# Kernel tuning notes

Measured on AMD Instinct MI355X. Metric: run time of the kernel, lower is better.

Reference implementation:

```python
import jax, jax.numpy as jnp
import numpy as np

H, HEADS, DH = 768, 8, 96
B, NPB = 32, 2048
N, E = B * NPB, B * NPB * 16
K_START = 3  # top-k query-similar start nodes per batch (min(3, nodes))
SCALE = np.float32(1.0 / np.sqrt(DH))


def _ln(x, g, b):
    m = x.mean(-1, keepdims=True)
    v = ((x - m) ** 2).mean(-1, keepdims=True)
    return (x - m) / jnp.sqrt(v + 1e-5) * g + b


def setup_inputs() -> dict:
    key = jax.random.key(0)
    ks = jax.random.split(key, 40)
    s = 0.02
    w = lambda k, sh: jax.random.normal(k, sh, jnp.float32) * s
    query = jax.random.normal(ks[0], (B, H), jnp.float32)
    node_features = jax.random.normal(ks[1], (N, H), jnp.float32)
    # edges only within a graph (contiguous blocks of NPB nodes per batch element)
    bvec = jax.random.randint(ks[2], (E,), 0, B)
    src = bvec * NPB + jax.random.randint(ks[3], (E,), 0, NPB)
    dst = bvec * NPB + jax.random.randint(ks[4], (E,), 0, NPB)
    edge_index = jnp.stack([src, dst]).astype(jnp.int32)
    batch_indices = jnp.repeat(jnp.arange(B, dtype=jnp.int32), NPB)
    inp = dict(query=query, node_features=node_features,
               edge_index=edge_index, batch_indices=batch_indices)
    # GraphReader params: query_projection, MHA in/out proj, LayerNorm
    inp.update(gr_wq=w(ks[5], (H, H)), gr_bq=jnp.zeros((H,)),
               gr_aq_w=w(ks[6], (H, H)), gr_aq_b=jnp.zeros((H,)),
               gr_ak_w=w(ks[7], (H, H)), gr_ak_b=jnp.zeros((H,)),
               gr_av_w=w(ks[8], (H, H)), gr_av_b=jnp.zeros((H,)),
               gr_ao_w=w(ks[9], (H, H)), gr_ao_b=jnp.zeros((H,)),
               gr_ln_g=jnp.ones((H,)), gr_ln_b=jnp.zeros((H,)))
    # PathFinder params: query/node projections, 2-layer path_aggregator, LayerNorm
    inp.update(pf_wq=w(ks[10], (H, H)), pf_bq=jnp.zeros((H,)),
               pf_wn=w(ks[11], (H, H)), pf_bn=jnp.zeros((H,)),
               pf_a1_w=w(ks[12], (H, H)), pf_a1_b=jnp.zeros((H,)),
               pf_a2_w=w(ks[13], (H, H)), pf_a2_b=jnp.zeros((H,)),
               pf_ln_g=jnp.ones((H,)), pf_ln_b=jnp.zeros((H,)))
    # ReasoningFusion (gate) params
    inp.update(fu_gw=w(ks[14], (3 * H, H)), fu_gb=jnp.zeros((H,)),
               fu_pw=w(ks[15], (3 * H, H)), fu_pb=jnp.zeros((H,)),
               fu_ln_g=jnp.ones((H,)), fu_ln_b=jnp.zeros((H,)))
    return inp


def reference(query, node_features, edge_index, batch_indices,
              gr_wq, gr_bq, gr_aq_w, gr_aq_b, gr_ak_w, gr_ak_b, gr_av_w, gr_av_b,
              gr_ao_w, gr_ao_b, gr_ln_g, gr_ln_b,
              pf_wq, pf_bq, pf_wn, pf_bn, pf_a1_w, pf_a1_b, pf_a2_w, pf_a2_b,
              pf_ln_g, pf_ln_b,
              fu_gw, fu_gb, fu_pw, fu_pb, fu_ln_g, fu_ln_b):
    node_b = jnp.arange(B)[:, None] == batch_indices[None, :]  # [B, N] per-batch mask

    # --- GraphReader: single-query masked multi-head attention over each graph ---
    qp = query @ gr_wq + gr_bq
    q = (qp @ gr_aq_w + gr_aq_b).reshape(B, HEADS, DH)
    k = (node_features @ gr_ak_w + gr_ak_b).reshape(N, HEADS, DH)
    v = (node_features @ gr_av_w + gr_av_b).reshape(N, HEADS, DH)
    scores = jnp.einsum('bhd,nhd->bhn', q, k) * SCALE
    scores = jnp.where(node_b[:, None, :], scores, -1e30)
    attn = jax.nn.softmax(scores, axis=-1)
    ctx = jnp.einsum('bhn,nhd->bhd', attn, v).reshape(B, H) @ gr_ao_w + gr_ao_b
    graph_repr = _ln(ctx, gr_ln_g, gr_ln_b)

    # --- PathFinder: top-3 cosine-similar starts, first BFS neighbor per start ---
    qp2 = query @ pf_wq + pf_bq
    nproj = node_features @ pf_wn + pf_bn
    qn = jnp.maximum(jnp.linalg.norm(qp2, axis=-1), 1e-8)
    nn_ = jnp.maximum(jnp.linalg.norm(nproj, axis=-1), 1e-8)
    sim = (qp2 @ nproj.T) / (qn[:, None] * nn_[None, :])
    sim = jnp.where(node_b, sim, -1e30)
    _, starts = jax.lax.top_k(sim, K_START)  # [B, 3] global node ids

    src, dst = edge_index[0], edge_index[1]
    intra = batch_indices[src] == batch_indices[dst]  # BFS keeps same-graph edges
    eids = jnp.where(intra, jnp.arange(E, dtype=jnp.int32), E)
    tgt = jnp.where(intra, src, N)
    # first outgoing edge per node in edge order == first BFS path (start, nbr)
    first_edge = jnp.full((N + 1,), E, jnp.int32).at[tgt].min(eids)[:N]
    has_nb = first_edge < E
    nbr = dst[jnp.minimum(first_edge, E - 1)]

    p_valid = has_nb[starts]  # [B, 3]
    # path length == max_hops (2) -> mean of the two node features (raw features)
    p_feat = (node_features[starts] + node_features[nbr[starts]]) * 0.5  # [B,3,H]
    cnt = p_valid.sum(-1)
    mean_paths = (p_feat * p_valid[..., None].astype(p_feat.dtype)).sum(1) \
                 / jnp.maximum(cnt, 1).astype(p_feat.dtype)[:, None]
    agg = jax.nn.relu(mean_paths @ pf_a1_w + pf_a1_b) @ pf_a2_w + pf_a2_b
    # fallback: mean of projected nodes of the graph when no path exists
    seg_sum = jax.ops.segment_sum(nproj, batch_indices, num_segments=B)
    seg_cnt = jax.ops.segment_sum(jnp.ones((N,), jnp.float32), batch_indices, num_segments=B)
    batch_mean = seg_sum / jnp.maximum(seg_cnt, 1.0)[:, None]
    path_repr = _ln(jnp.where((cnt > 0)[:, None], agg, batch_mean), pf_ln_g, pf_ln_b)

    # --- ReasoningFusion (gate) ---
    comb = jnp.concatenate([query, graph_repr, path_repr], axis=-1)  # [B, 3H]
    gate = jax.nn.sigmoid(comb @ fu_gw + fu_gb)
    fused = comb @ fu_pw + fu_pb
    return _ln(gate * fused, fu_ln_g, fu_ln_b)
```

## Files before the change

### kernel.cpp

```cpp
#include <hip/hip_runtime.h>
#include <hip/hip_bf16.h>

#define WB 32
#define WNPB 2048
#define WN 65536
#define WH 768
#define WHEADS 8
#define WDH 96
#define WE 1048576
#define WH3 2304
#define SCALE_QK 0.10206207261596577f

typedef float f32x4 __attribute__((ext_vector_type(4)));
typedef short bf16x8 __attribute__((ext_vector_type(8)));

__device__ __forceinline__ unsigned short f2bf(float x){
  __hip_bfloat16 h = __float2bfloat16(x);
  return *reinterpret_cast<unsigned short*>(&h);
}
__device__ __forceinline__ float bf2f(unsigned short u){
  __hip_bfloat16 h; *reinterpret_cast<unsigned short*>(&h) = u;
  return __bfloat162float(h);
}

__device__ __forceinline__ float wave_sum64(float v){
  #pragma unroll
  for(int o=32;o;o>>=1) v += __shfl_xor(v,o,64);
  return v;
}
__device__ __forceinline__ float block_sum256(float v, float* red){
  v = wave_sum64(v);
  __syncthreads();
  if((threadIdx.x&63)==0) red[threadIdx.x>>6]=v;
  __syncthreads();
  return red[0]+red[1]+red[2]+red[3];
}
__device__ __forceinline__ float block_max256(float v, float* red){
  #pragma unroll
  for(int o=32;o;o>>=1) v = fmaxf(v,__shfl_xor(v,o,64));
  __syncthreads();
  if((threadIdx.x&63)==0) red[threadIdx.x>>6]=v;
  __syncthreads();
  return fmaxf(fmaxf(red[0],red[1]),fmaxf(red[2],red[3]));
}

__global__ __launch_bounds__(256) void k_init(float* wnf, float* meannf,
                                              int* firstedge, int* cntb){
  int t = blockIdx.x*256+threadIdx.x;
  if(t < WB*WHEADS*WH) wnf[t]=0.f;
  if(t < WB*WH) meannf[t]=0.f;
  if(t < WN) firstedge[t]=WE;
  if(t < WB) cntb[t]=0;
}

__global__ __launch_bounds__(256) void k_prepw(const float* __restrict__ wn,
    unsigned short* __restrict__ th, unsigned short* __restrict__ tl){
  __shared__ float tile[64][68];
  int kt = blockIdx.x, nt = blockIdx.y, t = threadIdx.x;
  {
    int r = t>>2, q = t&3;
    const float4* src = (const float4*)(wn + (size_t)(kt*64 + r)*WH + nt*64 + q*16);
    float4 v0=src[0], v1=src[1], v2=src[2], v3=src[3];
    float* d = &tile[r][q*16];
    d[0]=v0.x; d[1]=v0.y; d[2]=v0.z; d[3]=v0.w;
    d[4]=v1.x; d[5]=v1.y; d[6]=v1.z; d[7]=v1.w;
    d[8]=v2.x; d[9]=v2.y; d[10]=v2.z; d[11]=v2.w;
    d[12]=v3.x; d[13]=v3.y; d[14]=v3.z; d[15]=v3.w;
  }
  __syncthreads();
  {
    int n = t>>2, q = t&3;
    #pragma unroll
    for(int e=0;e<16;++e){
      int kl = q*16 + e;
      float x = tile[kl][n];
      unsigned short h = f2bf(x);
      unsigned short l = f2bf(x - bf2f(h));
      size_t di = (size_t)(nt*64 + n)*WH + kt*64 + kl;
      th[di] = h; tl[di] = l;
    }
  }
}

__global__ __launch_bounds__(256) void k_gemm32(
    const float* __restrict__ A, const float* __restrict__ W,
    const float* __restrict__ bias, float* __restrict__ C,
    int relu, const int* __restrict__ cntb){
  __shared__ float a_t[WH*32];
  int t = threadIdx.x;
  for(int idx=t; idx<WH*32; idx+=256){
    int b = idx & 31, i = idx >> 5;
    float v = A[(size_t)b*WH + i];
    if(cntb){ int c = cntb[b]; v *= 1.f/(float)(c>1?c:1); }
    a_t[i*32 + b] = v;
  }
  __syncthreads();
  int jl = t & 63, bg = t >> 6;
  int j = blockIdx.x*64 + jl;
  float acc[8];
  #pragma unroll
  for(int k=0;k<8;++k) acc[k]=0.f;
  #pragma unroll 4
  for(int i=0;i<WH;++i){
    float w = W[(size_t)i*WH + j];
    const float4* ap = (const float4*)&a_t[i*32 + bg*8];
    float4 a0 = ap[0], a1 = ap[1];
    acc[0]+=a0.x*w; acc[1]+=a0.y*w; acc[2]+=a0.z*w; acc[3]+=a0.w*w;
    acc[4]+=a1.x*w; acc[5]+=a1.y*w; acc[6]+=a1.z*w; acc[7]+=a1.w*w;
  }
  float bj = bias? bias[j] : 0.f;
  #pragma unroll
  for(int bb=0;bb<8;++bb){
    float v = acc[bb] + bj;
    if(relu) v = fmaxf(v, 0.f);
    C[(size_t)(bg*8+bb)*WH + j] = v;
  }
}

__global__ __launch_bounds__(256) void k_gemm32t(
    const float* __restrict__ A, const float* __restrict__ W,
    float* __restrict__ C){
  __shared__ float a_t[WH*32];
  int t = threadIdx.x;
  for(int idx=t; idx<WH*32; idx+=256){
    int b = idx & 31, i = idx >> 5;
    a_t[i*32 + b] = A[(size_t)b*WH + i];
  }
  __syncthreads();
  int il = t & 63, bg = t >> 6;
  int i = blockIdx.x*64 + il;
  const float4* Wr = (const float4*)(W + (size_t)i*WH);
  float acc[8];
  #pragma unroll
  for(int k=0;k<8;++k) acc[k]=0.f;
  #pragma unroll 2
  for(int j4=0;j4<WH/4;++j4){
    float4 wv = Wr[j4];
    float ws[4] = {wv.x, wv.y, wv.z, wv.w};
    #pragma unroll
    for(int c=0;c<4;++c){
      const float4* ap = (const float4*)&a_t[(j4*4+c)*32 + bg*8];
      float4 a0 = ap[0], a1 = ap[1];
      float w = ws[c];
      acc[0]+=a0.x*w; acc[1]+=a0.y*w; acc[2]+=a0.z*w; acc[3]+=a0.w*w;
      acc[4]+=a1.x*w; acc[5]+=a1.y*w; acc[6]+=a1.z*w; acc[7]+=a1.w*w;
    }
  }
  #pragma unroll
  for(int bb=0;bb<8;++bb) C[(size_t)(bg*8+bb)*WH + i] = acc[bb];
}

__global__ __launch_bounds__(256) void k_qkvec(const float* __restrict__ q,
    const float* __restrict__ akw, const float* __restrict__ akb,
    float* __restrict__ qkvec, float* __restrict__ sconst){
  __shared__ float qlds[800];
  int b=blockIdx.y, ic=blockIdx.x, t=threadIdx.x;
  for(int idx=t; idx<WH; idx+=256){
    int h2 = idx/WDH, d = idx - h2*WDH;
    qlds[h2*100 + d] = q[(size_t)b*WH + idx];
  }
  __syncthreads();
  int il=t>>3, h=t&7;
  int i=ic*32+il;
  const float4* wr4 = (const float4*)(akw + (size_t)i*WH + h*WDH);
  float acc=0.f;
  #pragma unroll
  for(int u=0;u<WDH/4;++u){
    float4 w = wr4[u];
    const float4* qv4 = (const float4*)&qlds[h*100 + u*4];
    float4 qv = qv4[0];
    acc += w.x*qv.x + w.y*qv.y + w.z*qv.z + w.w*qv.w;
  }
  qkvec[((size_t)b*WH+i)*WHEADS + h] = acc;
  if(ic==0 && il==0){
    float sc=0.f;
    for(int d=0;d<WDH;++d) sc += qlds[h*100+d]*akb[h*WDH+d];
    sconst[b*WHEADS+h]=sc;
  }
}

__global__ __launch_bounds__(256) void k_qmisc(const float* __restrict__ qp2,
    const float* __restrict__ pbn, float* __restrict__ nconst, float* __restrict__ qn){
  __shared__ float red[4];
  int b=blockIdx.x, t=threadIdx.x;
  float s1=0.f,s2=0.f;
  for(int i=t;i<WH;i+=256){ float v=qp2[(size_t)b*WH+i]; s1+=v*pbn[i]; s2+=v*v; }
  s1=block_sum256(s1,red);
  s2=block_sum256(s2,red);
  if(t==0){ nconst[b]=s1; qn[b]=fmaxf(sqrtf(s2),1e-8f); }
}

__global__ __launch_bounds__(512) void k_normM(
    const float* __restrict__ nf, const uint4* __restrict__ wnTh,
    const uint4* __restrict__ wnTl, const float* __restrict__ bn,
    float* __restrict__ nnout){
  __shared__ uint4 Ah[128*8], Al[128*8];
  __shared__ uint4 Bh[256*8], Bl[256*8];
  __shared__ float sqred[128];
  int t = threadIdx.x, lane = t & 63, wid = t >> 6;
  int wr = wid >> 2, wc = wid & 3;
  int l15 = lane & 15, lg = lane >> 4;
  int r0 = blockIdx.x * 128;
  if(t < 128) sqred[t] = 0.f;
  float sqr[4][4];
  #pragma unroll
  for(int mi=0;mi<4;++mi)
    #pragma unroll
    for(int r=0;r<4;++r) sqr[mi][r]=0.f;

  for(int ct=0; ct<3; ++ct){
    f32x4 acc[4][4];
    #pragma unroll
    for(int mi=0;mi<4;++mi)
      #pragma unroll
      for(int ni=0;ni<4;++ni) acc[mi][ni] = (f32x4){0.f,0.f,0.f,0.f};

    for(int kt=0; kt<12; ++kt){
      __syncthreads();
      {
        int r = t >> 2, q = t & 3;
        const float4* src = (const float4*)(nf + (size_t)(r0 + r)*WH + kt*64 + q*16);
        float4 v0=src[0], v1=src[1], v2=src[2], v3=src[3];
        float vals[16] = {v0.x,v0.y,v0.z,v0.w, v1.x,v1.y,v1.z,v1.w,
                          v2.x,v2.y,v2.z,v2.w, v3.x,v3.y,v3.z,v3.w};
        unsigned int hd[8], ld_[8];
        #pragma unroll
        for(int e=0;e<8;++e){
          float x0 = vals[2*e], x1 = vals[2*e+1];
          unsigned short h0 = f2bf(x0), h1 = f2bf(x1);
          unsigned short l0 = f2bf(x0 - bf2f(h0)), l1 = f2bf(x1 - bf2f(h1));
          hd[e] = (unsigned)h0 | ((unsigned)h1 << 16);
          ld_[e] = (unsigned)l0 | ((unsigned)l1 << 16);
        }
        int sw = r & 7;
        uint4 uh0; uh0.x=hd[0]; uh0.y=hd[1]; uh0.z=hd[2]; uh0.w=hd[3];
        uint4 uh1; uh1.x=hd[4]; uh1.y=hd[5]; uh1.z=hd[6]; uh1.w=hd[7];
        uint4 ul0; ul0.x=ld_[0]; ul0.y=ld_[1]; ul0.z=ld_[2]; ul0.w=ld_[3];
        uint4 ul1; ul1.x=ld_[4]; ul1.y=ld_[5]; ul1.z=ld_[6]; ul1.w=ld_[7];
        Ah[r*8 + ((2*q  ) ^ sw)] = uh0;
        Ah[r*8 + ((2*q+1) ^ sw)] = uh1;
        Al[r*8 + ((2*q  ) ^ sw)] = ul0;
        Al[r*8 + ((2*q+1) ^ sw)] = ul1;
      }
      {
        int n = t >> 1, hh = t & 1;
        size_t gi = ((size_t)(ct*256 + n)*WH + kt*64 + hh*32) >> 3;
        int sw = n & 7;
        uint4 b0 = wnTh[gi], b1 = wnTh[gi+1], b2 = wnTh[gi+2], b3 = wnTh[gi+3];
        Bh[n*8 + ((4*hh  ) ^ sw)] = b0;
        Bh[n*8 + ((4*hh+1) ^ sw)] = b1;
        Bh[n*8 + ((4*hh+2) ^ sw)] = b2;
        Bh[n*8 + ((4*hh+3) ^ sw)] = b3;
        uint4 c0 = wnTl[gi], c1 = wnTl[gi+1], c2 = wnTl[gi+2], c3 = wnTl[gi+3];
        Bl[n*8 + ((4*hh  ) ^ sw)] = c0;
        Bl[n*8 + ((4*hh+1) ^ sw)] = c1;
        Bl[n*8 + ((4*hh+2) ^ sw)] = c2;
        Bl[n*8 + ((4*hh+3) ^ sw)] = c3;
      }
      __syncthreads();
      #pragma unroll
      for(int ks=0; ks<2; ++ks){
        bf16x8 ah[4], al_[4], bh[4], bl_[4];
        #pragma unroll
        for(int mi=0;mi<4;++mi){
          int row = wr*64 + mi*16 + l15;
          int u = (ks*4 + lg) ^ (row & 7);
          ah[mi]  = ((const bf16x8*)Ah)[row*8 + u];
          al_[mi] = ((const bf16x8*)Al)[row*8 + u];
        }
        #pragma unroll
        for(int ni=0;ni<4;++ni){
          int row = wc*64 + ni*16 + l15;
          int u = (ks*4 + lg) ^ (row & 7);
          bh[ni]  = ((const bf16x8*)Bh)[row*8 + u];
          bl_[ni] = ((const bf16x8*)Bl)[row*8 + u];
        }
        #pragma unroll
        for(int mi=0;mi<4;++mi)
          #pragma unroll
          for(int ni=0;ni<4;++ni){
            acc[mi][ni] = __builtin_amdgcn_mfma_f32_16x16x32_bf16(ah[mi],  bh[ni],  acc[mi][ni], 0,0,0);
            acc[mi][ni] = __builtin_amdgcn_mfma_f32_16x16x32_bf16(ah[mi],  bl_[ni], acc[mi][ni], 0,0,0);
            acc[mi][ni] = __builtin_amdgcn_mfma_f32_16x16x32_bf16(al_[mi], bh[ni],  acc[mi][ni], 0,0,0);
          }
      }
    }
    #pragma unroll
    for(int ni=0;ni<4;++ni){
      int col = ct*256 + wc*64 + ni*16 + l15;
      float bj = bn[col];
      #pragma unroll
      for(int mi=0;mi<4;++mi)
        #pragma unroll
        for(int r=0;r<4;++r){
          float v = acc[mi][ni][r] + bj;
          sqr[mi][r] += v*v;
        }
    }
  }
  #pragma unroll
  for(int mi=0;mi<4;++mi)
    #pragma unroll
    for(int r=0;r<4;++r){
      float v = sqr[mi][r];
      v += __shfl_xor(v, 1, 64);
      v += __shfl_xor(v, 2, 64);
      v += __shfl_xor(v, 4, 64);
      v += __shfl_xor(v, 8, 64);
      sqr[mi][r] = v;
    }
  if(l15 == 0){
    #pragma unroll
    for(int mi=0;mi<4;++mi)
      #pragma unroll
      for(int r=0;r<4;++r){
        int row = wr*64 + mi*16 + lg*4 + r;
        atomicAdd(&sqred[row], sqr[mi][r]);
      }
  }
  __syncthreads();
  if(t < 128) nnout[r0 + t] = fmaxf(sqrtf(sqred[t]), 1e-8f);
}

__global__ __launch_bounds__(256) void k_node1(
    const float* __restrict__ nf, const int* __restrict__ bidx,
    const float* __restrict__ qkvec, const float* __restrict__ wq2,
    const float* __restrict__ sconst, const float* __restrict__ nconst,
    float* __restrict__ s_out, float* __restrict__ numer,
    float* __restrict__ meannf, int* __restrict__ cntb){
  __shared__ float m_lds[4][WH];
  int lane = threadIdx.x&63, w = threadIdx.x>>6;
  int n0 = blockIdx.x*64;
  int b = bidx[n0];
  const float* qkb = qkvec + (size_t)b*WH*WHEADS;
  const float4* wqb4 = (const float4*)(wq2 + (size_t)b*WH);
  float sc[8];
  #pragma unroll
  for(int h=0;h<8;++h) sc[h]=sconst[b*WHEADS+h];
  float ncst = nconst[b];
  float macc[12];
  #pragma unroll
  for(int i=0;i<12;++i) macc[i]=0.f;
  for(int q_=0;q_<16;++q_){
    int n = n0 + w*16 + q_;
    const float4* nfr = (const float4*)(nf + (size_t)n*WH);
    float acc[8]; float anu=0.f;
    #pragma unroll
    for(int h=0;h<8;++h) acc[h]=0.f;
    #pragma unroll
    for(int tt=0;tt<3;++tt){
      int i4 = lane + 64*tt;
      float4 xv = nfr[i4];
      float4 wv = wqb4[i4];
      const float4* qk4 = (const float4*)(qkb + (size_t)i4*32);
      float xs[4]={xv.x,xv.y,xv.z,xv.w};
      float ws[4]={wv.x,wv.y,wv.z,wv.w};
      #pragma unroll
      for(int u=0;u<4;++u){
        float x = xs[u];
        float4 qa = qk4[2*u], qb = qk4[2*u+1];
        acc[0]+=x*qa.x; acc[1]+=x*qa.y; acc[2]+=x*qa.z; acc[3]+=x*qa.w;
        acc[4]+=x*qb.x; acc[5]+=x*qb.y; acc[6]+=x*qb.z; acc[7]+=x*qb.w;
        anu += x*ws[u];
        macc[tt*4+u]+=x;
      }
    }
    #pragma unroll
    for(int h=0;h<8;++h) acc[h]=wave_sum64(acc[h]);
    anu = wave_sum64(anu);
    if(lane==0){
      #pragma unroll
      for(int h=0;h<8;++h) s_out[(size_t)n*8+h] = SCALE_QK*(acc[h]+sc[h]);
      numer[n] = anu + ncst;
    }
  }
  #pragma unroll
  for(int tt=0;tt<3;++tt){
    #pragma unroll
    for(int u=0;u<4;++u) m_lds[w][4*lane+256*tt+u]=macc[tt*4+u];
  }
  __syncthreads();
  for(int i=threadIdx.x;i<WH;i+=256)
    atomicAdd(&meannf[(size_t)b*WH+i],
              m_lds[0][i]+m_lds[1][i]+m_lds[2][i]+m_lds[3][i]);
  if(threadIdx.x==0) atomicAdd(&cntb[b],64);
}

__global__ __launch_bounds__(256) void k_stats(const float* __restrict__ s,
    float* __restrict__ rowmax, float* __restrict__ rowinv){
  __shared__ float red[4];
  int b = blockIdx.x>>3, h = blockIdx.x&7;
  const float* sp = s + (size_t)b*WNPB*8 + h;
  float mx=-3e38f;
  for(int i=threadIdx.x;i<WNPB;i+=256) mx=fmaxf(mx, sp[(size_t)i*8]);
  mx = block_max256(mx, red);
  float se=0.f;
  for(int i=threadIdx.x;i<WNPB;i+=256) se += __expf(sp[(size_t)i*8]-mx);
  se = block_sum256(se, red);
  if(threadIdx.x==0){ rowmax[blockIdx.x]=mx; rowinv[blockIdx.x]=1.f/se; }
}

__global__ __launch_bounds__(256) void k_node2(
    const float* __restrict__ nf, const float* __restrict__ s,
    const float* __restrict__ rowmax, const float* __restrict__ rowinv,
    float* __restrict__ wnf){
  __shared__ float p_lds[128*8];
  int b = blockIdx.x >> 4, ch = blockIdx.x & 15;
  int t = threadIdx.x;
  int n0 = b*WNPB + ch*128;
  for(int idx=t; idx<1024; idx+=256){
    int nl = idx >> 3, h = idx & 7;
    p_lds[idx] = __expf(s[(size_t)(n0+nl)*8 + h] - rowmax[b*8+h]) * rowinv[b*8+h];
  }
  __syncthreads();
  float racc[24];
  #pragma unroll
  for(int i=0;i<24;++i) racc[i]=0.f;
  const float* nfb = nf + (size_t)n0*WH;
  #pragma unroll 2
  for(int m=0;m<128;++m){
    float x0 = nfb[(size_t)m*WH + t];
    float x1 = nfb[(size_t)m*WH + t + 256];
    float x2 = nfb[(size_t)m*WH + t + 512];
    const float* pm = p_lds + m*8;
    #pragma unroll
    for(int h=0;h<8;++h){
      float p = pm[h];
      racc[h*3+0] += p*x0; racc[h*3+1] += p*x1; racc[h*3+2] += p*x2;
    }
  }
  float* wb = wnf + (size_t)b*WHEADS*WH;
  #pragma unroll
  for(int h=0;h<8;++h){
    atomicAdd(&wb[h*WH + t],       racc[h*3+0]);
    atomicAdd(&wb[h*WH + t + 256], racc[h*3+1]);
    atomicAdd(&wb[h*WH + t + 512], racc[h*3+2]);
  }
}

__global__ __launch_bounds__(256) void k_ctx(const float* __restrict__ wnf,
    const float* __restrict__ W, const float* __restrict__ bias,
    float* __restrict__ C){
  __shared__ float a_lds[WHEADS*WH];
  int b = blockIdx.x, t = threadIdx.x;
  const float* Ar = wnf + (size_t)b*WHEADS*WH;
  for(int i=t;i<WHEADS*WH;i+=256) a_lds[i]=Ar[i];
  __syncthreads();
  #pragma unroll
  for(int jo=0;jo<3;++jo){
    int j = jo*256+t;
    const float* ap = a_lds + (j/WDH)*WH;
    const float* wp = W + j;
    float acc=0.f;
    #pragma unroll 4
    for(int i=0;i<WH;++i) acc += ap[i]*wp[(size_t)i*WH];
    C[(size_t)b*WH+j] = acc + bias[j];
  }
}

__device__ __forceinline__ void top3_insert(float v, int i, float* tv, int* ti){
  if (v>tv[0] || (v==tv[0] && i<ti[0])){
    tv[2]=tv[1]; ti[2]=ti[1]; tv[1]=tv[0]; ti[1]=ti[0]; tv[0]=v; ti[0]=i;
  } else if (v>tv[1] || (v==tv[1] && i<ti[1])){
    tv[2]=tv[1]; ti[2]=ti[1]; tv[1]=v; ti[1]=i;
  } else if (v>tv[2] || (v==tv[2] && i<ti[2])){
    tv[2]=v; ti[2]=i;
  }
}
__global__ __launch_bounds__(256) void k_top3(const float* __restrict__ numer,
    const float* __restrict__ nrm, const float* __restrict__ qn,
    int* __restrict__ starts){
  __shared__ float sv[256][3];
  __shared__ int   si[256][3];
  int b=blockIdx.x, t=threadIdx.x;
  float qv = qn[b];
  float tv[3]={-3e38f,-3e38f,-3e38f};
  int   ti[3]={0x7fffffff,0x7fffffff,0x7fffffff};
  for(int u=t;u<WNPB;u+=256){
    int n=b*WNPB+u;
    float v = numer[n]/(qv*nrm[n]);
    top3_insert(v,n,tv,ti);
  }
  sv[t][0]=tv[0];sv[t][1]=tv[1];sv[t][2]=tv[2];
  si[t][0]=ti[0];si[t][1]=ti[1];si[t][2]=ti[2];
  __syncthreads();
  for(int st=128;st;st>>=1){
    if(t<st){
      #pragma unroll
      for(int k=0;k<3;++k) top3_insert(sv[t+st][k], si[t+st][k], tv, ti);
      sv[t][0]=tv[0];sv[t][1]=tv[1];sv[t][2]=tv[2];
      si[t][0]=ti[0];si[t][1]=ti[1];si[t][2]=ti[2];
    }
    __syncthreads();
  }
  if(t<3) starts[b*3+t]=si[0][t];
}

__global__ __launch_bounds__(256) void k_edges(const int* __restrict__ ei,
    const int* __restrict__ bidx, int* __restrict__ firstedge,
    float* __restrict__ fzero){
  int e = blockIdx.x*256+threadIdx.x;
  if(e < 2*WB*WH) fzero[e] = 0.f;
  if(e<WE){
    int s=ei[e], d=ei[WE+e];
    if(bidx[s]==bidx[d]) atomicMin(&firstedge[s], e);
  }
}

__global__ __launch_bounds__(256) void k_path(const int* __restrict__ starts,
    const int* __restrict__ firstedge, const int* __restrict__ dst,
    const float* __restrict__ nf, float* __restrict__ mpaths,
    int* __restrict__ cntpath){
  int b=blockIdx.x;
  int sl[3], nl[3], vl[3]; int cnt=0;
  #pragma unroll
  for(int k=0;k<3;++k){
    int st = starts[b*3+k];
    int fe = firstedge[st];
    int valid = fe<WE;
    sl[k]=st; nl[k]= valid? dst[fe] : 0; vl[k]=valid; cnt+=valid;
  }
  float inv = 1.f/(float)(cnt>1?cnt:1);
  for(int j=threadIdx.x;j<WH;j+=256){
    float acc=0.f;
    #pragma unroll
    for(int k=0;k<3;++k)
      if(vl[k]) acc += 0.5f*(nf[(size_t)sl[k]*WH+j] + nf[(size_t)nl[k]*WH+j]);
    mpaths[(size_t)b*WH+j]=acc*inv;
  }
  if(threadIdx.x==0) cntpath[b]=cnt;
}

__global__ __launch_bounds__(256) void k_selln(const float* __restrict__ agg,
    const float* __restrict__ bmean, const int* __restrict__ cntpath,
    const float* __restrict__ g, const float* __restrict__ bb,
    float* __restrict__ out){
  __shared__ float red[4];
  int b=blockIdx.x, t=threadIdx.x;
  const float* src = agg;
  if(cntpath && cntpath[b]<=0) src = bmean;
  src += (size_t)b*WH;
  float x[3];
  #pragma unroll
  for(int jo=0;jo<3;++jo) x[jo]=src[jo*256+t];
  float s = block_sum256(x[0]+x[1]+x[2], red);
  float m = s*(1.f/768.f);
  float d0=x[0]-m,d1=x[1]-m,d2=x[2]-m;
  float v = block_sum256(d0*d0+d1*d1+d2*d2, red)*(1.f/768.f);
  float inv = rsqrtf(v+1e-5f);
  #pragma unroll
  for(int jo=0;jo<3;++jo){ int j=jo*256+t;
    out[(size_t)b*WH+j]=(x[jo]-m)*inv*g[j]+bb[j]; }
}

__global__ __launch_bounds__(256) void k_fuse_mm(
    const float* __restrict__ query, const float* __restrict__ graphr,
    const float* __restrict__ pathr, const float* __restrict__ gw,
    const float* __restrict__ pw, float* __restrict__ facc){
  __shared__ float c_t[576*32];
  int t = threadIdx.x;
  int jt = blockIdx.x, kc = blockIdx.y;
  for(int idx=t; idx<576*32; idx+=256){
    int b = idx & 31, ii = idx >> 5;
    int gi = kc*576 + ii;
    float v;
    if(gi < WH)        v = query [(size_t)b*WH + gi];
    else if(gi < 2*WH) v = graphr[(size_t)b*WH + gi - WH];
    else               v = pathr [(size_t)b*WH + gi - 2*WH];
    c_t[ii*32 + b] = v;
  }
  __syncthreads();
  int jl = t & 63, bg = t >> 6;
  int j = jt*64 + jl;
  float ag[8], ap[8];
  #pragma unroll
  for(int k=0;k<8;++k){ ag[k]=0.f; ap[k]=0.f; }
  #pragma unroll 2
  for(int ii=0;ii<576;++ii){
    size_t wi = (size_t)(kc*576 + ii)*WH + j;
    float wg = gw[wi], wp = pw[wi];
    const float4* cp = (const float4*)&c_t[ii*32 + bg*8];
    float4 a0 = cp[0], a1 = cp[1];
    ag[0]+=a0.x*wg; ag[1]+=a0.y*wg; ag[2]+=a0.z*wg; ag[3]+=a0.w*wg;
    ag[4]+=a1.x*wg; ag[5]+=a1.y*wg; ag[6]+=a1.z*wg; ag[7]+=a1.w*wg;
    ap[0]+=a0.x*wp; ap[1]+=a0.y*wp; ap[2]+=a0.z*wp; ap[3]+=a0.w*wp;
    ap[4]+=a1.x*wp; ap[5]+=a1.y*wp; ap[6]+=a1.z*wp; ap[7]+=a1.w*wp;
  }
  #pragma unroll
  for(int bb=0;bb<8;++bb){
    atomicAdd(&facc[(size_t)(bg*8+bb)*WH + j], ag[bb]);
    atomicAdd(&facc[(size_t)WB*WH + (size_t)(bg*8+bb)*WH + j], ap[bb]);
  }
}

__global__ __launch_bounds__(256) void k_fuse_ep(const float* __restrict__ facc,
    const float* __restrict__ gb, const float* __restrict__ pb,
    const float* __restrict__ g, const float* __restrict__ bb,
    float* __restrict__ out){
  __shared__ float red[4];
  int b=blockIdx.x, t=threadIdx.x;
  float vals[3];
  #pragma unroll
  for(int jo=0;jo<3;++jo){
    int j=jo*256+t;
    float ag = facc[(size_t)b*WH + j] + gb[j];
    float ap = facc[(size_t)WB*WH + (size_t)b*WH + j] + pb[j];
    float sg = 1.f/(1.f+__expf(-ag));
    vals[jo]=sg*ap;
  }
  float s = block_sum256(vals[0]+vals[1]+vals[2], red);
  float m = s*(1.f/768.f);
  float d0=vals[0]-m,d1=vals[1]-m,d2=vals[2]-m;
  float v = block_sum256(d0*d0+d1*d1+d2*d2, red)*(1.f/768.f);
  float inv = rsqrtf(v+1e-5f);
  #pragma unroll
  for(int jo=0;jo<3;++jo){
    int j=jo*256+t;
    out[(size_t)b*WH+j] = (vals[jo]-m)*inv*g[j]+bb[j];
  }
}

extern "C" void kernel_launch(void* const* d_in, const int* in_sizes, int n_in,
                              void* d_out, int out_size, void* d_ws, size_t ws_size,
                              hipStream_t stream){
  const float* query  =(const float*)d_in[0];
  const float* nf     =(const float*)d_in[1];
  const int*   ei     =(const int*)  d_in[2];
  const int*   bidx   =(const int*)  d_in[3];
  const float* gr_wq  =(const float*)d_in[4];
  const float* gr_bq  =(const float*)d_in[5];
  const float* gr_aq_w=(const float*)d_in[6];
  const float* gr_aq_b=(const float*)d_in[7];
  const float* gr_ak_w=(const float*)d_in[8];
  const float* gr_ak_b=(const float*)d_in[9];
  const float* gr_av_w=(const float*)d_in[10];
  const float* gr_av_b=(const float*)d_in[11];
  const float* gr_ao_w=(const float*)d_in[12];
  const float* gr_ao_b=(const float*)d_in[13];
  const float* gr_ln_g=(const float*)d_in[14];
  const float* gr_ln_b=(const float*)d_in[15];
  const float* pf_wq  =(const float*)d_in[16];
  const float* pf_bq  =(const float*)d_in[17];
  const float* pf_wn  =(const float*)d_in[18];
  const float* pf_bn  =(const float*)d_in[19];
  const float* pf_a1_w=(const float*)d_in[20];
  const float* pf_a1_b=(const float*)d_in[21];
  const float* pf_a2_w=(const float*)d_in[22];
  const float* pf_a2_b=(const float*)d_in[23];
  const float* pf_ln_g=(const float*)d_in[24];
  const float* pf_ln_b=(const float*)d_in[25];
  const float* fu_gw  =(const float*)d_in[26];
  const float* fu_gb  =(const float*)d_in[27];
  const float* fu_pw  =(const float*)d_in[28];
  const float* fu_pb  =(const float*)d_in[29];
  const float* fu_ln_g=(const float*)d_in[30];
  const float* fu_ln_b=(const float*)d_in[31];
  float* out =(float*)d_out;

  float* w=(float*)d_ws;
  size_t o=0;
  float* sregion=w+o; o+=(size_t)WN*WHEADS + WN;
  float* s      = sregion;
  float* numer  = sregion + (size_t)WN*WHEADS;
  unsigned short* wnTh = (unsigned short*)sregion;
  unsigned short* wnTl = ((unsigned short*)sregion) + (size_t)WH*WH;
  float* qp     =w+o; o+=WB*WH;
  float* qp2    =w+o; o+=WB*WH;
  float* q      =w+o; o+=WB*WH;
  float* wq2    =w+o; o+=WB*WH;
  float* qkvec  =w+o; o+=(size_t)WB*WH*WHEADS;
  float* ctxo   = qkvec;
  float* fuse_acc = qkvec + WB*WH;
  float* sconst =w+o; o+=WB*WHEADS;
  float* nconst =w+o; o+=64;
  float* qn     =w+o; o+=64;
  float* nrm    =w+o; o+=WN;
  float* meannf =w+o; o+=WB*WH;
  float* rowmax =w+o; o+=WB*WHEADS;
  float* rowinv =w+o; o+=WB*WHEADS;
  float* wnf    =w+o; o+=(size_t)WB*WHEADS*WH;
  float* ctx    =w+o; o+=WB*WH;
  float* graphr =w+o; o+=WB*WH;
  float* mpaths =w+o; o+=WB*WH;
  float* t1     =w+o; o+=WB*WH;
  float* agg    =w+o; o+=WB*WH;
  float* bmean  =w+o; o+=WB*WH;
  float* pathr  =w+o; o+=WB*WH;
  int* iw=(int*)(w+o);
  int* firstedge=iw; iw+=WN;
  int* cntb     =iw; iw+=64;
  int* starts   =iw; iw+=128;
  int* cntpath  =iw; iw+=64;

  dim3 blk(256);
  k_init   <<<768,blk,0,stream>>>(wnf, meannf, firstedge, cntb);
  k_prepw  <<<dim3(12,12),blk,0,stream>>>(pf_wn, wnTh, wnTl);
  k_gemm32 <<<12,blk,0,stream>>>(query, gr_wq, gr_bq, qp, 0, nullptr);
  k_gemm32 <<<12,blk,0,stream>>>(query, pf_wq, pf_bq, qp2, 0, nullptr);
  k_gemm32 <<<12,blk,0,stream>>>(qp, gr_aq_w, gr_aq_b, q, 0, nullptr);
  k_gemm32t<<<12,blk,0,stream>>>(qp2, pf_wn, wq2);
  k_qkvec  <<<dim3(24,32),blk,0,stream>>>(q, gr_ak_w, gr_ak_b, qkvec, sconst);
  k_qmisc  <<<WB,blk,0,stream>>>(qp2, pf_bn, nconst, qn);
  k_normM  <<<WN/128,dim3(512),0,stream>>>(nf, (const uint4*)wnTh, (const uint4*)wnTl, pf_bn, nrm);
  k_node1  <<<WN/64,blk,0,stream>>>(nf, bidx, qkvec, wq2, sconst, nconst, s, numer, meannf, cntb);
  k_stats  <<<WB*WHEADS,blk,0,stream>>>(s, rowmax, rowinv);
  k_node2  <<<WB*16,blk,0,stream>>>(nf, s, rowmax, rowinv, wnf);
  k_ctx    <<<WB,blk,0,stream>>>(wnf, gr_av_w, gr_av_b, ctx);
  k_gemm32 <<<12,blk,0,stream>>>(ctx, gr_ao_w, gr_ao_b, ctxo, 0, nullptr);
  k_selln  <<<WB,blk,0,stream>>>(ctxo, ctxo, nullptr, gr_ln_g, gr_ln_b, graphr);
  k_top3   <<<WB,blk,0,stream>>>(numer, nrm, qn, starts);
  k_edges  <<<WE/256,blk,0,stream>>>(ei, bidx, firstedge, fuse_acc);
  k_path   <<<WB,blk,0,stream>>>(starts, firstedge, ei+WE, nf, mpaths, cntpath);
  k_gemm32 <<<12,blk,0,stream>>>(mpaths, pf_a1_w, pf_a1_b, t1, 1, nullptr);
  k_gemm32 <<<12,blk,0,stream>>>(t1, pf_a2_w, pf_a2_b, agg, 0, nullptr);
  k_gemm32 <<<12,blk,0,stream>>>(meannf, pf_wn, pf_bn, bmean, 0, cntb);
  k_selln  <<<WB,blk,0,stream>>>(agg, bmean, cntpath, pf_ln_g, pf_ln_b, pathr);
  k_fuse_mm<<<dim3(12,4),blk,0,stream>>>(query, graphr, pathr, fu_gw, fu_pw, fuse_acc);
  k_fuse_ep<<<WB,blk,0,stream>>>(fuse_acc, fu_gb, fu_pb, fu_ln_g, fu_ln_b, out);
}
```

Measured before the change: 2.051 ms.

## Merge small GEMM launches, restructure node2 reduction, shrink normM K-tile, transpose qkvec

```diff
diff --git a/kernel.cpp b/kernel.cpp
--- a/kernel.cpp
+++ b/kernel.cpp
@@ -44,10 +44,8 @@
   return fmaxf(fmaxf(red[0],red[1]),fmaxf(red[2],red[3]));
 }
 
-__global__ __launch_bounds__(256) void k_init(float* wnf, float* meannf,
-                                              int* firstedge, int* cntb){
+__global__ __launch_bounds__(256) void k_init(float* meannf, int* firstedge, int* cntb){
   int t = blockIdx.x*256+threadIdx.x;
-  if(t < WB*WHEADS*WH) wnf[t]=0.f;
   if(t < WB*WH) meannf[t]=0.f;
   if(t < WN) firstedge[t]=WE;
   if(t < WB) cntb[t]=0;
@@ -82,11 +80,10 @@
   }
 }
 
-__global__ __launch_bounds__(256) void k_gemm32(
+__device__ __forceinline__ void gemm32_body(
     const float* __restrict__ A, const float* __restrict__ W,
     const float* __restrict__ bias, float* __restrict__ C,
-    int relu, const int* __restrict__ cntb){
-  __shared__ float a_t[WH*32];
+    int relu, const int* __restrict__ cntb, float* a_t){
   int t = threadIdx.x;
   for(int idx=t; idx<WH*32; idx+=256){
     int b = idx & 31, i = idx >> 5;
@@ -116,6 +113,22 @@
     C[(size_t)(bg*8+bb)*WH + j] = v;
   }
 }
+__global__ __launch_bounds__(256) void k_gemm32(
+    const float* __restrict__ A, const float* __restrict__ W,
+    const float* __restrict__ bias, float* __restrict__ C,
+    int relu, const int* __restrict__ cntb){
+  __shared__ float a_t[WH*32];
+  gemm32_body(A,W,bias,C,relu,cntb,a_t);
+}
+__global__ __launch_bounds__(256) void k_gemm32d(
+    const float* __restrict__ A0, const float* __restrict__ W0,
+    const float* __restrict__ b0, float* __restrict__ C0, int r0_, const int* c0,
+    const float* __restrict__ A1, const float* __restrict__ W1,
+    const float* __restrict__ b1, float* __restrict__ C1, int r1_, const int* c1){
+  __shared__ float a_t[WH*32];
+  if(blockIdx.y==0) gemm32_body(A0,W0,b0,C0,r0_,c0,a_t);
+  else              gemm32_body(A1,W1,b1,C1,r1_,c1,a_t);
+}
 
 __global__ __launch_bounds__(256) void k_gemm32t(
     const float* __restrict__ A, const float* __restrict__ W,
@@ -152,7 +165,7 @@
 
 __global__ __launch_bounds__(256) void k_qkvec(const float* __restrict__ q,
     const float* __restrict__ akw, const float* __restrict__ akb,
-    float* __restrict__ qkvec, float* __restrict__ sconst){
+    float* __restrict__ qkT, float* __restrict__ sconst){
   __shared__ float qlds[800];
   int b=blockIdx.y, ic=blockIdx.x, t=threadIdx.x;
   for(int idx=t; idx<WH; idx+=256){
@@ -167,11 +180,10 @@
   #pragma unroll
   for(int u=0;u<WDH/4;++u){
     float4 w = wr4[u];
-    const float4* qv4 = (const float4*)&qlds[h*100 + u*4];
-    float4 qv = qv4[0];
+    float4 qv = *(const float4*)&qlds[h*100 + u*4];
     acc += w.x*qv.x + w.y*qv.y + w.z*qv.z + w.w*qv.w;
   }
-  qkvec[((size_t)b*WH+i)*WHEADS + h] = acc;
+  qkT[((size_t)b*WHEADS+h)*WH + i] = acc;
   if(ic==0 && il==0){
     float sc=0.f;
     for(int d=0;d<WDH;++d) sc += qlds[h*100+d]*akb[h*WDH+d];
@@ -194,8 +206,8 @@
     const float* __restrict__ nf, const uint4* __restrict__ wnTh,
     const uint4* __restrict__ wnTl, const float* __restrict__ bn,
     float* __restrict__ nnout){
-  __shared__ uint4 Ah[128*8], Al[128*8];
-  __shared__ uint4 Bh[256*8], Bl[256*8];
+  __shared__ uint4 Ah[128*4], Al[128*4];
+  __shared__ uint4 Bh[256*4], Bl[256*4];
   __shared__ float sqred[128];
   int t = threadIdx.x, lane = t & 63, wid = t >> 6;
   int wr = wid >> 2, wc = wid & 3;
@@ -208,6 +220,9 @@
     #pragma unroll
     for(int r=0;r<4;++r) sqr[mi][r]=0.f;
 
+  int sa_r = t >> 2, sa_q = t & 3;
+  int sb_n = t >> 1, sb_h = t & 1;
+
   for(int ct=0; ct<3; ++ct){
     f32x4 acc[4][4];
     #pragma unroll
@@ -215,75 +230,63 @@
       #pragma unroll
       for(int ni=0;ni<4;++ni) acc[mi][ni] = (f32x4){0.f,0.f,0.f,0.f};
 
-    for(int kt=0; kt<12; ++kt){
+    for(int kt=0; kt<24; ++kt){
       __syncthreads();
       {
-        int r = t >> 2, q = t & 3;
-        const float4* src = (const float4*)(nf + (size_t)(r0 + r)*WH + kt*64 + q*16);
-        float4 v0=src[0], v1=src[1], v2=src[2], v3=src[3];
-        float vals[16] = {v0.x,v0.y,v0.z,v0.w, v1.x,v1.y,v1.z,v1.w,
-                          v2.x,v2.y,v2.z,v2.w, v3.x,v3.y,v3.z,v3.w};
-        unsigned int hd[8], ld_[8];
+        const float4* src = (const float4*)(nf + (size_t)(r0 + sa_r)*WH + kt*32 + sa_q*8);
+        float4 v0=src[0], v1=src[1];
+        float vals[8] = {v0.x,v0.y,v0.z,v0.w, v1.x,v1.y,v1.z,v1.w};
+        unsigned int hd[4], ld_[4];
         #pragma unroll
-        for(int e=0;e<8;++e){
+        for(int e=0;e<4;++e){
           float x0 = vals[2*e], x1 = vals[2*e+1];
           unsigned short h0 = f2bf(x0), h1 = f2bf(x1);
           unsigned short l0 = f2bf(x0 - bf2f(h0)), l1 = f2bf(x1 - bf2f(h1));
           hd[e] = (unsigned)h0 | ((unsigned)h1 << 16);
           ld_[e] = (unsigned)l0 | ((unsigned)l1 << 16);
         }
-        int sw = r & 7;
-        uint4 uh0; uh0.x=hd[0]; uh0.y=hd[1]; uh0.z=hd[2]; uh0.w=hd[3];
-        uint4 uh1; uh1.x=hd[4]; uh1.y=hd[5]; uh1.z=hd[6]; uh1.w=hd[7];
-        uint4 ul0; ul0.x=ld_[0]; ul0.y=ld_[1]; ul0.z=ld_[2]; ul0.w=ld_[3];
-        uint4 ul1; ul1.x=ld_[4]; ul1.y=ld_[5]; ul1.z=ld_[6]; ul1.w=ld_[7];
-        Ah[r*8 + ((2*q  ) ^ sw)] = uh0;
-        Ah[r*8 + ((2*q+1) ^ sw)] = uh1;
-        Al[r*8 + ((2*q  ) ^ sw)] = ul0;
-        Al[r*8 + ((2*q+1) ^ sw)] = ul1;
+        int sw = sa_r & 3;
+        uint4 uh; uh.x=hd[0]; uh.y=hd[1]; uh.z=hd[2]; uh.w=hd[3];
+        uint4 ul; ul.x=ld_[0]; ul.y=ld_[1]; ul.z=ld_[2]; ul.w=ld_[3];
+        Ah[sa_r*4 + (sa_q ^ sw)] = uh;
+        Al[sa_r*4 + (sa_q ^ sw)] = ul;
       }
       {
-        int n = t >> 1, hh = t & 1;
-        size_t gi = ((size_t)(ct*256 + n)*WH + kt*64 + hh*32) >> 3;
-        int sw = n & 7;
-        uint4 b0 = wnTh[gi], b1 = wnTh[gi+1], b2 = wnTh[gi+2], b3 = wnTh[gi+3];
-        Bh[n*8 + ((4*hh  ) ^ sw)] = b0;
-        Bh[n*8 + ((4*hh+1) ^ sw)] = b1;
-        Bh[n*8 + ((4*hh+2) ^ sw)] = b2;
-        Bh[n*8 + ((4*hh+3) ^ sw)] = b3;
-        uint4 c0 = wnTl[gi], c1 = wnTl[gi+1], c2 = wnTl[gi+2], c3 = wnTl[gi+3];
-        Bl[n*8 + ((4*hh  ) ^ sw)] = c0;
-        Bl[n*8 + ((4*hh+1) ^ sw)] = c1;
-        Bl[n*8 + ((4*hh+2) ^ sw)] = c2;
-        Bl[n*8 + ((4*hh+3) ^ sw)] = c3;
+        size_t gi = (size_t)(ct*256 + sb_n)*96 + kt*4 + sb_h*2;
+        int sw = sb_n & 3;
+        uint4 b0 = wnTh[gi], b1 = wnTh[gi+1];
+        Bh[sb_n*4 + ((2*sb_h  ) ^ sw)] = b0;
+        Bh[sb_n*4 + ((2*sb_h+1) ^ sw)] = b1;
+        uint4 c0 = wnTl[gi], c1 = wnTl[gi+1];
+        Bl[sb_n*4 + ((2*sb_h  ) ^ sw)] = c0;
+        Bl[sb_n*4 + ((2*sb_h+1) ^ sw)] = c1;
       }
       __syncthreads();
-      #pragma unroll
-      for(int ks=0; ks<2; ++ks){
-        bf16x8 ah[4], al_[4], bh[4], bl_[4];
-        #pragma unroll
-        for(int mi=0;mi<4;++mi){
-          int row = wr*64 + mi*16 + l15;
-          int u = (ks*4 + lg) ^ (row & 7);
-          ah[mi]  = ((const bf16x8*)Ah)[row*8 + u];
-          al_[mi] = ((const bf16x8*)Al)[row*8 + u];
-        }
+      bf16x8 ah[4], al_[4], bh[4], bl_[4];
+      #pragma unroll
+      for(int mi=0;mi<4;++mi){
+        int row = wr*64 + mi*16 + l15;
+        int u = lg ^ (row & 3);
+        ah[mi]  = ((const bf16x8*)Ah)[row*4 + u];
+        al_[mi] = ((const bf16x8*)Al)[row*4 + u];
+      }
+      #pragma unroll
+      for(int ni=0;ni<4;++ni){
+        int row = wc*64 + ni*16 + l15;
+        int u = lg ^ (row & 3);
+        bh[ni]  = ((const bf16x8*)Bh)[row*4 + u];
+        bl_[ni] = ((const bf16x8*)Bl)[row*4 + u];
+      }
+      __builtin_amdgcn_s_setprio(1);
+      #pragma unroll
+      for(int mi=0;mi<4;++mi)
         #pragma unroll
         for(int ni=0;ni<4;++ni){
-          int row = wc*64 + ni*16 + l15;
-          int u = (ks*4 + lg) ^ (row & 7);
-          bh[ni]  = ((const bf16x8*)Bh)[row*8 + u];
-          bl_[ni] = ((const bf16x8*)Bl)[row*8 + u];
+          acc[mi][ni] = __builtin_amdgcn_mfma_f32_16x16x32_bf16(ah[mi],  bh[ni],  acc[mi][ni], 0,0,0);
+          acc[mi][ni] = __builtin_amdgcn_mfma_f32_16x16x32_bf16(ah[mi],  bl_[ni], acc[mi][ni], 0,0,0);
+          acc[mi][ni] = __builtin_amdgcn_mfma_f32_16x16x32_bf16(al_[mi], bh[ni],  acc[mi][ni], 0,0,0);
         }
-        #pragma unroll
-        for(int mi=0;mi<4;++mi)
-          #pragma unroll
-          for(int ni=0;ni<4;++ni){
-            acc[mi][ni] = __builtin_amdgcn_mfma_f32_16x16x32_bf16(ah[mi],  bh[ni],  acc[mi][ni], 0,0,0);
-            acc[mi][ni] = __builtin_amdgcn_mfma_f32_16x16x32_bf16(ah[mi],  bl_[ni], acc[mi][ni], 0,0,0);
-            acc[mi][ni] = __builtin_amdgcn_mfma_f32_16x16x32_bf16(al_[mi], bh[ni],  acc[mi][ni], 0,0,0);
-          }
-      }
+      __builtin_amdgcn_s_setprio(0);
     }
     #pragma unroll
     for(int ni=0;ni<4;++ni){
@@ -323,16 +326,16 @@
 }
 
 __global__ __launch_bounds__(256) void k_node1(
-    const float* __restrict__ nf, const int* __restrict__ bidx,
-    const float* __restrict__ qkvec, const float* __restrict__ wq2,
+    const float* __restrict__ nf,
+    const float* __restrict__ qkT, const float* __restrict__ wq2,
     const float* __restrict__ sconst, const float* __restrict__ nconst,
     float* __restrict__ s_out, float* __restrict__ numer,
     float* __restrict__ meannf, int* __restrict__ cntb){
   __shared__ float m_lds[4][WH];
   int lane = threadIdx.x&63, w = threadIdx.x>>6;
   int n0 = blockIdx.x*64;
-  int b = bidx[n0];
-  const float* qkb = qkvec + (size_t)b*WH*WHEADS;
+  int b = n0 >> 11;
+  const float4* qkb4 = (const float4*)(qkT + (size_t)b*WHEADS*WH);
   const float4* wqb4 = (const float4*)(wq2 + (size_t)b*WH);
   float sc[8];
   #pragma unroll
@@ -352,18 +355,13 @@
       int i4 = lane + 64*tt;
       float4 xv = nfr[i4];
       float4 wv = wqb4[i4];
-      const float4* qk4 = (const float4*)(qkb + (size_t)i4*32);
-      float xs[4]={xv.x,xv.y,xv.z,xv.w};
-      float ws[4]={wv.x,wv.y,wv.z,wv.w};
-      #pragma unroll
-      for(int u=0;u<4;++u){
-        float x = xs[u];
-        float4 qa = qk4[2*u], qb = qk4[2*u+1];
-        acc[0]+=x*qa.x; acc[1]+=x*qa.y; acc[2]+=x*qa.z; acc[3]+=x*qa.w;
-        acc[4]+=x*qb.x; acc[5]+=x*qb.y; acc[6]+=x*qb.z; acc[7]+=x*qb.w;
-        anu += x*ws[u];
-        macc[tt*4+u]+=x;
+      #pragma unroll
+      for(int h=0;h<8;++h){
+        float4 qv = qkb4[h*192 + i4];
+        acc[h] += xv.x*qv.x + xv.y*qv.y + xv.z*qv.z + xv.w*qv.w;
       }
+      anu += xv.x*wv.x + xv.y*wv.y + xv.z*wv.z + xv.w*wv.w;
+      macc[tt*4+0]+=xv.x; macc[tt*4+1]+=xv.y; macc[tt*4+2]+=xv.z; macc[tt*4+3]+=xv.w;
     }
     #pragma unroll
     for(int h=0;h<8;++h) acc[h]=wave_sum64(acc[h]);
@@ -404,37 +402,45 @@
     const float* __restrict__ nf, const float* __restrict__ s,
     const float* __restrict__ rowmax, const float* __restrict__ rowinv,
     float* __restrict__ wnf){
-  __shared__ float p_lds[128*8];
-  int b = blockIdx.x >> 4, ch = blockIdx.x & 15;
+  __shared__ float p_lds[WNPB*8];
+  int b = blockIdx.y, ds = blockIdx.x;
   int t = threadIdx.x;
-  int n0 = b*WNPB + ch*128;
-  for(int idx=t; idx<1024; idx+=256){
-    int nl = idx >> 3, h = idx & 7;
-    p_lds[idx] = __expf(s[(size_t)(n0+nl)*8 + h] - rowmax[b*8+h]) * rowinv[b*8+h];
-  }
-  __syncthreads();
-  float racc[24];
-  #pragma unroll
-  for(int i=0;i<24;++i) racc[i]=0.f;
-  const float* nfb = nf + (size_t)n0*WH;
-  #pragma unroll 2
-  for(int m=0;m<128;++m){
-    float x0 = nfb[(size_t)m*WH + t];
-    float x1 = nfb[(size_t)m*WH + t + 256];
-    float x2 = nfb[(size_t)m*WH + t + 512];
-    const float* pm = p_lds + m*8;
+  float rm[8], ri[8];
+  #pragma unroll
+  for(int h=0;h<8;++h){ rm[h]=rowmax[b*8+h]; ri[h]=rowinv[b*8+h]; }
+  for(int idx=t; idx<WNPB*8; idx+=256){
+    int nl = idx>>3, h = idx&7;
+    p_lds[idx] = __expf(s[((size_t)b*WNPB+nl)*8+h] - rm[h]) * ri[h];
+  }
+  __syncthreads();
+  int cg = t & 15, ng = t >> 4;
+  const float* nfb = nf + (size_t)b*WNPB*WH + ds*64 + cg*4;
+  f32x4 acc8[8];
+  #pragma unroll
+  for(int h=0;h<8;++h) acc8[h]=(f32x4){0.f,0.f,0.f,0.f};
+  for(int m=ng; m<WNPB; m+=16){
+    float4 x = *(const float4*)(nfb + (size_t)m*WH);
+    const float* pm = &p_lds[m*8];
     #pragma unroll
     for(int h=0;h<8;++h){
       float p = pm[h];
-      racc[h*3+0] += p*x0; racc[h*3+1] += p*x1; racc[h*3+2] += p*x2;
-    }
-  }
-  float* wb = wnf + (size_t)b*WHEADS*WH;
-  #pragma unroll
-  for(int h=0;h<8;++h){
-    atomicAdd(&wb[h*WH + t],       racc[h*3+0]);
-    atomicAdd(&wb[h*WH + t + 256], racc[h*3+1]);
-    atomicAdd(&wb[h*WH + t + 512], racc[h*3+2]);
+      acc8[h][0] += p*x.x; acc8[h][1] += p*x.y;
+      acc8[h][2] += p*x.z; acc8[h][3] += p*x.w;
+    }
+  }
+  __syncthreads();
+  f32x4* red4 = (f32x4*)p_lds;
+  #pragma unroll
+  for(int h=0;h<8;++h) red4[(ng*16+cg)*8 + h] = acc8[h];
+  __syncthreads();
+  if(t < 128){
+    int cg2 = t&15, h2 = t>>4;
+    f32x4 sum = (f32x4){0.f,0.f,0.f,0.f};
+    #pragma unroll
+    for(int g=0;g<16;++g){ f32x4 v = red4[(g*16+cg2)*8+h2];
+      sum[0]+=v[0]; sum[1]+=v[1]; sum[2]+=v[2]; sum[3]+=v[3]; }
+    float* dst = wnf + ((size_t)b*WHEADS+h2)*WH + ds*64 + cg2*4;
+    dst[0]=sum[0]; dst[1]=sum[1]; dst[2]=sum[2]; dst[3]=sum[3];
   }
 }
 
@@ -467,9 +473,11 @@
     tv[2]=v; ti[2]=i;
   }
 }
-__global__ __launch_bounds__(256) void k_top3(const float* __restrict__ numer,
+__global__ __launch_bounds__(256) void k_tp(const float* __restrict__ numer,
     const float* __restrict__ nrm, const float* __restrict__ qn,
-    int* __restrict__ starts){
+    const int* __restrict__ firstedge, const int* __restrict__ dst,
+    const float* __restrict__ nf, float* __restrict__ mpaths,
+    int* __restrict__ cntpath){
   __shared__ float sv[256][3];
   __shared__ int   si[256][3];
   int b=blockIdx.x, t=threadIdx.x;
@@ -493,42 +501,33 @@
     }
     __syncthreads();
   }
-  if(t<3) starts[b*3+t]=si[0][t];
+  int sl[3], nl[3], vl[3]; int cnt=0;
+  #pragma unroll
+  for(int k=0;k<3;++k){
+    int st = si[0][k];
+    int fe = firstedge[st];
+    int valid = fe<WE;
+    sl[k]=st; nl[k]= valid? dst[fe] : 0; vl[k]=valid; cnt+=valid;
+  }
+  float inv = 1.f/(float)(cnt>1?cnt:1);
+  for(int j=t;j<WH;j+=256){
+    float acc=0.f;
+    #pragma unroll
+    for(int k=0;k<3;++k)
+      if(vl[k]) acc += 0.5f*(nf[(size_t)sl[k]*WH+j] + nf[(size_t)nl[k]*WH+j]);
+    mpaths[(size_t)b*WH+j]=acc*inv;
+  }
+  if(t==0) cntpath[b]=cnt;
 }
 
 __global__ __launch_bounds__(256) void k_edges(const int* __restrict__ ei,
-    const int* __restrict__ bidx, int* __restrict__ firstedge,
-    float* __restrict__ fzero){
+    int* __restrict__ firstedge, float* __restrict__ fzero){
   int e = blockIdx.x*256+threadIdx.x;
   if(e < 2*WB*WH) fzero[e] = 0.f;
   if(e<WE){
     int s=ei[e], d=ei[WE+e];
-    if(bidx[s]==bidx[d]) atomicMin(&firstedge[s], e);
-  }
-}
-
-__global__ __launch_bounds__(256) void k_path(const int* __restrict__ starts,
-    const int* __restrict__ firstedge, const int* __restrict__ dst,
-    const float* __restrict__ nf, float* __restrict__ mpaths,
-    int* __restrict__ cntpath){
-  int b=blockIdx.x;
-  int sl[3], nl[3], vl[3]; int cnt=0;
-  #pragma unroll
-  for(int k=0;k<3;++k){
-    int st = starts[b*3+k];
-    int fe = firstedge[st];
-    int valid = fe<WE;
-    sl[k]=st; nl[k]= valid? dst[fe] : 0; vl[k]=valid; cnt+=valid;
-  }
-  float inv = 1.f/(float)(cnt>1?cnt:1);
-  for(int j=threadIdx.x;j<WH;j+=256){
-    float acc=0.f;
-    #pragma unroll
-    for(int k=0;k<3;++k)
-      if(vl[k]) acc += 0.5f*(nf[(size_t)sl[k]*WH+j] + nf[(size_t)nl[k]*WH+j]);
-    mpaths[(size_t)b*WH+j]=acc*inv;
-  }
-  if(threadIdx.x==0) cntpath[b]=cnt;
+    if((s>>11)==(d>>11)) atomicMin(&firstedge[s], e);
+  }
 }
 
 __global__ __launch_bounds__(256) void k_selln(const float* __restrict__ agg,
@@ -626,7 +625,6 @@
   const float* query  =(const float*)d_in[0];
   const float* nf     =(const float*)d_in[1];
   const int*   ei     =(const int*)  d_in[2];
-  const int*   bidx   =(const int*)  d_in[3];
   const float* gr_wq  =(const float*)d_in[4];
   const float* gr_bq  =(const float*)d_in[5];
   const float* gr_aq_w=(const float*)d_in[6];
@@ -668,9 +666,9 @@
   float* qp2    =w+o; o+=WB*WH;
   float* q      =w+o; o+=WB*WH;
   float* wq2    =w+o; o+=WB*WH;
-  float* qkvec  =w+o; o+=(size_t)WB*WH*WHEADS;
-  float* ctxo   = qkvec;
-  float* fuse_acc = qkvec + WB*WH;
+  float* qkvecT =w+o; o+=(size_t)WB*WH*WHEADS;
+  float* ctxo   = qkvecT;
+  float* fuse_acc = qkvecT + WB*WH;
   float* sconst =w+o; o+=WB*WHEADS;
   float* nconst =w+o; o+=64;
   float* qn     =w+o; o+=64;
@@ -689,31 +687,29 @@
   int* iw=(int*)(w+o);
   int* firstedge=iw; iw+=WN;
   int* cntb     =iw; iw+=64;
-  int* starts   =iw; iw+=128;
   int* cntpath  =iw; iw+=64;
 
   dim3 blk(256);
-  k_init   <<<768,blk,0,stream>>>(wnf, meannf, firstedge, cntb);
+  k_init   <<<256,blk,0,stream>>>(meannf, firstedge, cntb);
   k_prepw  <<<dim3(12,12),blk,0,stream>>>(pf_wn, wnTh, wnTl);
-  k_gemm32 <<<12,blk,0,stream>>>(query, gr_wq, gr_bq, qp, 0, nullptr);
-  k_gemm32 <<<12,blk,0,stream>>>(query, pf_wq, pf_bq, qp2, 0, nullptr);
+  k_gemm32d<<<dim3(12,2),blk,0,stream>>>(query, gr_wq, gr_bq, qp, 0, nullptr,
+                                         query, pf_wq, pf_bq, qp2, 0, nullptr);
   k_gemm32 <<<12,blk,0,stream>>>(qp, gr_aq_w, gr_aq_b, q, 0, nullptr);
   k_gemm32t<<<12,blk,0,stream>>>(qp2, pf_wn, wq2);
-  k_qkvec  <<<dim3(24,32),blk,0,stream>>>(q, gr_ak_w, gr_ak_b, qkvec, sconst);
+  k_qkvec  <<<dim3(24,32),blk,0,stream>>>(q, gr_ak_w, gr_ak_b, qkvecT, sconst);
   k_qmisc  <<<WB,blk,0,stream>>>(qp2, pf_bn, nconst, qn);
   k_normM  <<<WN/128,dim3(512),0,stream>>>(nf, (const uint4*)wnTh, (const uint4*)wnTl, pf_bn, nrm);
-  k_node1  <<<WN/64,blk,0,stream>>>(nf, bidx, qkvec, wq2, sconst, nconst, s, numer, meannf, cntb);
+  k_node1  <<<WN/64,blk,0,stream>>>(nf, qkvecT, wq2, sconst, nconst, s, numer, meannf, cntb);
   k_stats  <<<WB*WHEADS,blk,0,stream>>>(s, rowmax, rowinv);
-  k_node2  <<<WB*16,blk,0,stream>>>(nf, s, rowmax, rowinv, wnf);
+  k_node2  <<<dim3(12,WB),blk,0,stream>>>(nf, s, rowmax, rowinv, wnf);
   k_ctx    <<<WB,blk,0,stream>>>(wnf, gr_av_w, gr_av_b, ctx);
   k_gemm32 <<<12,blk,0,stream>>>(ctx, gr_ao_w, gr_ao_b, ctxo, 0, nullptr);
   k_selln  <<<WB,blk,0,stream>>>(ctxo, ctxo, nullptr, gr_ln_g, gr_ln_b, graphr);
-  k_top3   <<<WB,blk,0,stream>>>(numer, nrm, qn, starts);
-  k_edges  <<<WE/256,blk,0,stream>>>(ei, bidx, firstedge, fuse_acc);
-  k_path   <<<WB,blk,0,stream>>>(starts, firstedge, ei+WE, nf, mpaths, cntpath);
-  k_gemm32 <<<12,blk,0,stream>>>(mpaths, pf_a1_w, pf_a1_b, t1, 1, nullptr);
+  k_edges  <<<WE/256,blk,0,stream>>>(ei, firstedge, fuse_acc);
+  k_tp     <<<WB,blk,0,stream>>>(numer, nrm, qn, firstedge, ei+WE, nf, mpaths, cntpath);
+  k_gemm32d<<<dim3(12,2),blk,0,stream>>>(mpaths, pf_a1_w, pf_a1_b, t1, 1, nullptr,
+                                         meannf, pf_wn, pf_bn, bmean, 0, cntb);
   k_gemm32 <<<12,blk,0,stream>>>(t1, pf_a2_w, pf_a2_b, agg, 0, nullptr);
-  k_gemm32 <<<12,blk,0,stream>>>(meannf, pf_wn, pf_bn, bmean, 0, cntb);
   k_selln  <<<WB,blk,0,stream>>>(agg, bmean, cntpath, pf_ln_g, pf_ln_b, pathr);
   k_fuse_mm<<<dim3(12,4),blk,0,stream>>>(query, graphr, pathr, fu_gw, fu_pw, fuse_acc);
   k_fuse_ep<<<WB,blk,0,stream>>>(fuse_acc, fu_gb, fu_pb, fu_ln_g, fu_ln_b, out);
```

New measurement: 1.893 ms. -7.7%, faster.
